# Kernel optimization log

Hardware: AMD Instinct MI355X
Metric: run time of the kernel (lower is better)

Reference implementation:

```python
import jax, jax.numpy as jnp
import numpy as np

ALPHA = 0.2


def setup_inputs() -> dict:
    key = jax.random.key(0)
    k1, k2 = jax.random.split(key)
    x = jax.random.normal(k1, (32, 4096, 256), dtype=jnp.float32)
    mask = jax.random.randint(k2, (32, 4096), 0, 2, dtype=jnp.int32)
    return {"x": x, "mask": mask}


def _ema_scan(x, mask, alpha):
    # x: (B, T, D), mask: (B, T) int; recurrence along T via lax.scan.
    x_t = jnp.swapaxes(x, 0, 1)                     # (T, B, D)
    valid_t = mask.astype(x.dtype).T[..., None]     # (T, B, 1)
    ema0 = x_t[0]                                   # ema[:,0] = x[:,0] (mask not applied at t=0)

    def step(prev, inp):
        xt, vt = inp
        cand = (1.0 - alpha) * prev + alpha * xt
        new = cand * vt + prev * (1.0 - vt)         # gated carry-forward on invalid steps
        return new, new

    _, ema_rest = jax.lax.scan(step, ema0, (x_t[1:], valid_t[1:]))
    ema = jnp.concatenate([ema0[None], ema_rest], axis=0)  # (T, B, D)
    return jnp.swapaxes(ema, 0, 1)                  # (B, T, D)


def reference(x, mask):
    return _ema_scan(x, mask, ALPHA)
```

## Files before the change

kernel.cpp:

```cpp
#include <hip/hip_runtime.h>


constexpr int BATCH  = 32;
constexpr int TLEN   = 4096;
constexpr int DD     = 256;
constexpr int OLEN   = 512;
constexpr int WARM   = 128;
constexpr int CHUNKS = TLEN / OLEN;
constexpr int QTRS   = 4;
constexpr int NWAVE  = BATCH * CHUNKS * QTRS;
constexpr int WPB    = 4;
constexpr int NBLK   = NWAVE / WPB;

#define EMA_ALPHA 0.2f
#define EMA_OMA   0.8f

__device__ __forceinline__ void nt_store_f(float* dst, float v) {
    __builtin_nontemporal_store(v, dst);
}

__global__ __launch_bounds__(256)
void ema_wave(const float* __restrict__ x, const int* __restrict__ mask,
              float* __restrict__ out) {
    const int lane = threadIdx.x & 63;
    const int wave = blockIdx.x * WPB + (threadIdx.x >> 6);
    const int h = wave & (QTRS - 1);
    const int c = (wave >> 2) & (CHUNKS - 1);
    const int b = wave >> 5;

    int start = c * OLEN - WARM; if (start < 0) start = 0;
    const int tot    = c * OLEN + OLEN - start;
    const int nwin   = tot >> 6;
    const int outwin = nwin - OLEN / 64;
    const bool f0    = (c == 0);

    const int d = h * 64 + lane;
    const float* xp = x + ((size_t)b * TLEN + start) * DD + d;
    const int*   mp = mask + b * TLEN + start;
    float*       op = out + ((size_t)b * TLEN + c * OLEN) * DD + d;

    float s = 0.f;
    float xa[32], xb[32];
    float res[32];
    #pragma unroll
    for (int i = 0; i < 32; ++i) xa[i] = xp[(size_t)i * DD];

    auto window = [&](int win, bool isout, bool first) {
        const unsigned long long bal = __ballot(mp[win * 64 + lane] != 0);
        const int obase = win * 64 - (tot - OLEN);
        #pragma unroll
        for (int g = 0; g < 2; ++g) {
            {
                int qn = win * 64 + (g + 1) * 32;
                if (qn + 32 > tot) qn = tot - 32;
                float* dst = (g == 0) ? xb : xa;
                #pragma unroll
                for (int i = 0; i < 32; ++i) dst[i] = xp[(size_t)(qn + i) * DD];
            }
            const float* cur = (g == 0) ? xa : xb;
            #pragma unroll
            for (int i = 0; i < 32; ++i) {
                const int j = g * 32 + i;
                const bool bit = (bal >> j) & 1ull;
                float a  = bit ? EMA_OMA   : 1.0f;
                float cf = bit ? EMA_ALPHA : 0.0f;
                if (first && g == 0 && i == 0) { a = 0.0f; cf = 1.0f; }
                s = a * s + cf * cur[i];
                if (isout) res[i] = s;
            }
            if (isout) {
                #pragma unroll
                for (int i = 0; i < 32; ++i)
                    nt_store_f(&op[(size_t)(obase + g * 32 + i) * DD], res[i]);
            }
        }
    };

    int win = 0;
    for (; win < outwin; ++win) window(win, false, f0 && win == 0);
    for (; win < nwin;   ++win) window(win, true,  f0 && win == 0);
}

extern "C" void kernel_launch(void* const* d_in, const int* in_sizes, int n_in,
                              void* d_out, int out_size, void* d_ws, size_t ws_size,
                              hipStream_t stream) {
    const float* x  = (const float*)d_in[0];
    const int* mask = (const int*)d_in[1];
    float* out      = (float*)d_out;

    ema_wave<<<NBLK, 256, 0, stream>>>(x, mask, out);
}
```

Baseline: 49.24 us.

## Gate x loads on mask bits and deepen prefetch to four quarter-window buffers

When a timestep's mask bit is zero, the load now reads a single cached base address instead of that row, because the value is multiplied by zero in the recurrence. This removes roughly the masked fraction of x reads from DRAM traffic in this bandwidth-bound scan. The double-buffered loads are also replaced by four 32-step register buffers, so data is prefetched three quarter-windows ahead, with scheduling barriers between stages. This raises register pressure and may lower occupancy.

```diff
diff --git a/kernel.cpp b/kernel.cpp
--- a/kernel.cpp
+++ b/kernel.cpp
@@ -15,9 +15,45 @@
 #define EMA_ALPHA 0.2f
 #define EMA_OMA   0.8f
 
+typedef unsigned long long u64;
+typedef unsigned int u32;
+
 __device__ __forceinline__ void nt_store_f(float* dst, float v) {
     __builtin_nontemporal_store(v, dst);
 }
+
+#define PRE(GG, BUF, PB64)                                                   \
+    {                                                                        \
+        int qn = (GG) * 32;                                                  \
+        if (qn + 32 > tot) qn = tot - 32;                                    \
+        const u64 pb_ = (PB64);                                              \
+        _Pragma("unroll")                                                    \
+        for (int i = 0; i < 32; ++i) {                                       \
+            const float* pp =                                                \
+                ((pb_ >> i) & 1ull) ? &xp[(size_t)(qn + i) * DD] : xp;       \
+            BUF[i] = *pp;                                                    \
+        }                                                                    \
+        __builtin_amdgcn_sched_barrier(0);                                   \
+    }
+
+#define SCAN(BUF, PB32, FIRST, ISOUT, OB)                                    \
+    {                                                                        \
+        const u32 pb_ = (PB32);                                              \
+        _Pragma("unroll")                                                    \
+        for (int i = 0; i < 32; ++i) {                                       \
+            const bool bit = (pb_ >> i) & 1u;                                \
+            float a  = bit ? EMA_OMA   : 1.0f;                               \
+            float cf = bit ? EMA_ALPHA : 0.0f;                               \
+            if ((FIRST) && i == 0) { a = 0.0f; cf = 1.0f; }                  \
+            s = a * s + cf * BUF[i];                                         \
+            if (ISOUT) res[i] = s;                                           \
+        }                                                                    \
+        if (ISOUT) {                                                         \
+            _Pragma("unroll")                                                \
+            for (int i = 0; i < 32; ++i)                                     \
+                nt_store_f(&op[(size_t)((OB) + i) * DD], res[i]);            \
+        }                                                                    \
+    }
 
 __global__ __launch_bounds__(256)
 void ema_wave(const float* __restrict__ x, const int* __restrict__ mask,
@@ -40,45 +76,40 @@
     float*       op = out + ((size_t)b * TLEN + c * OLEN) * DD + d;
 
     float s = 0.f;
-    float xa[32], xb[32];
+    float q0[32], q1[32], q2[32], q3[32];
     float res[32];
-    #pragma unroll
-    for (int i = 0; i < 32; ++i) xa[i] = xp[(size_t)i * DD];
 
-    auto window = [&](int win, bool isout, bool first) {
-        const unsigned long long bal = __ballot(mp[win * 64 + lane] != 0);
-        const int obase = win * 64 - (tot - OLEN);
-        #pragma unroll
-        for (int g = 0; g < 2; ++g) {
-            {
-                int qn = win * 64 + (g + 1) * 32;
-                if (qn + 32 > tot) qn = tot - 32;
-                float* dst = (g == 0) ? xb : xa;
-                #pragma unroll
-                for (int i = 0; i < 32; ++i) dst[i] = xp[(size_t)(qn + i) * DD];
-            }
-            const float* cur = (g == 0) ? xa : xb;
-            #pragma unroll
-            for (int i = 0; i < 32; ++i) {
-                const int j = g * 32 + i;
-                const bool bit = (bal >> j) & 1ull;
-                float a  = bit ? EMA_OMA   : 1.0f;
-                float cf = bit ? EMA_ALPHA : 0.0f;
-                if (first && g == 0 && i == 0) { a = 0.0f; cf = 1.0f; }
-                s = a * s + cf * cur[i];
-                if (isout) res[i] = s;
-            }
-            if (isout) {
-                #pragma unroll
-                for (int i = 0; i < 32; ++i)
-                    nt_store_f(&op[(size_t)(obase + g * 32 + i) * DD], res[i]);
-            }
-        }
+    auto wb = [&](int wi) {
+        const int w = (wi < nwin) ? wi : (nwin - 1);
+        return __ballot(mp[w * 64 + lane] != 0);
     };
 
-    int win = 0;
-    for (; win < outwin; ++win) window(win, false, f0 && win == 0);
-    for (; win < nwin;   ++win) window(win, true,  f0 && win == 0);
+    u64 B0 = wb(0), B1 = wb(1);
+
+    PRE(0, q0, B0 | (f0 ? 1ull : 0ull));
+    PRE(1, q1, B0 >> 32);
+    PRE(2, q2, B1);
+
+    const int nsb = nwin >> 1;
+    for (int sb = 0; sb < nsb; ++sb) {
+        const int win    = 2 * sb;
+        const bool isout = (win >= outwin);
+        const bool first = f0 && (sb == 0);
+        const u64 B2 = wb(win + 2), B3 = wb(win + 3);
+        const int ob0 = win * 64 - (tot - OLEN);
+        const int ob1 = ob0 + 64;
+
+        PRE(win * 2 + 3, q3, B1 >> 32);
+        SCAN(q0, (u32)B0, first, isout, ob0);
+        PRE(win * 2 + 4, q0, B2);
+        SCAN(q1, (u32)(B0 >> 32), false, isout, ob0 + 32);
+        PRE(win * 2 + 5, q1, B2 >> 32);
+        SCAN(q2, (u32)B1, false, isout, ob1);
+        PRE(win * 2 + 6, q2, B3);
+        SCAN(q3, (u32)(B1 >> 32), false, isout, ob1 + 32);
+
+        B0 = B2; B1 = B3;
+    }
 }
 
 extern "C" void kernel_launch(void* const* d_in, const int* in_sizes, int n_in,
```

After: 40.33 us. -18.1%, faster.
